# Kernel optimization log

Measured on AMD Instinct MI355X. Metric: run time of the kernel, lower is better.

The kernel has to match this reference:

```python
import jax, jax.numpy as jnp
import numpy as np

B, N, M = 2, 1024, 512
D, H, DH = 1024, 16, 64          # features, heads, head dim (D == H*DH)
MID = H * DH
DC = 768                          # context_features
MULT = 4
EPS = 1e-5


def _ln(x, w, b):
    mu = jnp.mean(x, -1, keepdims=True)
    var = jnp.mean((x - mu) ** 2, -1, keepdims=True)
    return (x - mu) * jax.lax.rsqrt(var + EPS) * w + b


def _sincos(n, d):
    inv = 1.0 / (10000.0 ** (jnp.arange(0, d, 2, dtype=jnp.float32) / d))
    ang = jnp.arange(n, dtype=jnp.float32)[:, None] * inv[None, :]
    return jnp.sin(ang), jnp.cos(ang)


def _rope(x, sin, cos):
    # x: [B,H,N,DH]; sin/cos: [N, DH//2]; interleaved even/odd rotation
    s = sin[None, None]
    c = cos[None, None]
    xe = x[..., ::2]
    xo = x[..., 1::2]
    re = xe * c - xo * s
    ro = xe * s + xo * c
    return jnp.stack((re, ro), axis=-1).reshape(x.shape)


def _heads(t):
    b, n, _ = t.shape
    return t.reshape(b, n, H, DH).transpose(0, 2, 1, 3)


def _attn(xq, ctx, wq, wkv, wo, bo):
    q = _heads(xq @ wq)
    k, v = jnp.split(ctx @ wkv, 2, axis=-1)
    k = _heads(k)
    v = _heads(v)
    sq, cq = _sincos(q.shape[2], DH)
    sk, ck = _sincos(k.shape[2], DH)
    q = _rope(q, sq, cq)
    k = _rope(k, sk, ck)
    sim = jnp.einsum('bhnd,bhmd->bhnm', q, k) * (DH ** -0.5)
    a = jax.nn.softmax(sim, axis=-1)
    o = jnp.einsum('bhnm,bhmd->bhnd', a, v)
    o = o.transpose(0, 2, 1, 3).reshape(xq.shape[0], xq.shape[1], MID)
    return o @ wo + bo


def _adaln(x, c, lw, lb, gw, gb, bw, bb):
    g = (c @ gw + gb)[:, None, :]
    bt = (c @ bw + bb)[:, None, :]
    return _ln(x, lw, lb) * (1.0 + g) + bt


def setup_inputs() -> dict:
    ks = jax.random.split(jax.random.key(0), 24)
    s = 0.02
    inp = {
        'x': jax.random.normal(ks[0], (B, N, D), jnp.float32),
        'cond': jax.random.normal(ks[1], (B, D), jnp.float32),
        'context': jax.random.normal(ks[2], (B, M, DC), jnp.float32),
        # AdaLN (attn_mod) — reused for self- and cross-attention pre-norm
        'ln1_w': jnp.ones((D,), jnp.float32),
        'ln1_b': jnp.zeros((D,), jnp.float32),
        'g1_w': jax.random.normal(ks[3], (D, D), jnp.float32) * s,
        'g1_b': jnp.zeros((D,), jnp.float32),
        'b1_w': jax.random.normal(ks[4], (D, D), jnp.float32) * s,
        'b1_b': jnp.zeros((D,), jnp.float32),
        # AdaLN (ffn_mod)
        'ln2_w': jnp.ones((D,), jnp.float32),
        'ln2_b': jnp.zeros((D,), jnp.float32),
        'g2_w': jax.random.normal(ks[5], (D, D), jnp.float32) * s,
        'g2_b': jnp.zeros((D,), jnp.float32),
        'b2_w': jax.random.normal(ks[6], (D, D), jnp.float32) * s,
        'b2_b': jnp.zeros((D,), jnp.float32),
        # self-attention
        'sa_wq': jax.random.normal(ks[7], (D, MID), jnp.float32) * s,
        'sa_wkv': jax.random.normal(ks[8], (D, 2 * MID), jnp.float32) * s,
        'sa_wo': jax.random.normal(ks[9], (MID, D), jnp.float32) * s,
        'sa_bo': jnp.zeros((D,), jnp.float32),
        # cross-attention (context LayerNorm + projections)
        'ca_lnc_w': jnp.ones((DC,), jnp.float32),
        'ca_lnc_b': jnp.zeros((DC,), jnp.float32),
        'ca_wq': jax.random.normal(ks[10], (D, MID), jnp.float32) * s,
        'ca_wkv': jax.random.normal(ks[11], (DC, 2 * MID), jnp.float32) * s,
        'ca_wo': jax.random.normal(ks[12], (MID, D), jnp.float32) * s,
        'ca_bo': jnp.zeros((D,), jnp.float32),
        # FFN
        'ff_w1': jax.random.normal(ks[13], (D, MULT * D), jnp.float32) * s,
        'ff_b1': jnp.zeros((MULT * D,), jnp.float32),
        'ff_w2': jax.random.normal(ks[14], (MULT * D, D), jnp.float32) * s,
        'ff_b2': jnp.zeros((D,), jnp.float32),
    }
    return inp


def reference(x, cond, context,
              ln1_w, ln1_b, g1_w, g1_b, b1_w, b1_b,
              ln2_w, ln2_b, g2_w, g2_b, b2_w, b2_b,
              sa_wq, sa_wkv, sa_wo, sa_bo,
              ca_lnc_w, ca_lnc_b, ca_wq, ca_wkv, ca_wo, ca_bo,
              ff_w1, ff_b1, ff_w2, ff_b2):
    # self-attention with shared attn_mod AdaLN
    attn_in = _adaln(x, cond, ln1_w, ln1_b, g1_w, g1_b, b1_w, b1_b)
    x = _attn(attn_in, attn_in, sa_wq, sa_wkv, sa_wo, sa_bo) + x
    # cross-attention (attn_mod reused, context LayerNorm applied)
    cross_in = _adaln(x, cond, ln1_w, ln1_b, g1_w, g1_b, b1_w, b1_b)
    ctx_n = _ln(context, ca_lnc_w, ca_lnc_b)
    x = _attn(cross_in, ctx_n, ca_wq, ca_wkv, ca_wo, ca_bo) + x
    # FFN with ffn_mod AdaLN, exact GELU (torch default)
    ffn_in = _adaln(x, cond, ln2_w, ln2_b, g2_w, g2_b, b2_w, b2_b)
    h = jax.nn.gelu(ffn_in @ ff_w1 + ff_b1, approximate=False)
    x = h @ ff_w2 + ff_b2 + x
    return x
```

## Files before the change

kernel.cpp:

```cpp
#include <hip/hip_runtime.h>
#include <hip/hip_bf16.h>
#include <math.h>


typedef float f32x4 __attribute__((ext_vector_type(4)));
typedef __bf16 bf16x8 __attribute__((ext_vector_type(8)));
typedef __bf16 bf16x4 __attribute__((ext_vector_type(4)));
typedef __bf16 bf16x2 __attribute__((ext_vector_type(2)));

#define DEVI __device__ __forceinline__

DEVI void gload16(const void* g, void* l) {
  __builtin_amdgcn_global_load_lds((const __attribute__((address_space(1))) void*)g,
                                   (__attribute__((address_space(3))) void*)l, 16, 0, 0);
}

struct WtDesc {
  const float* src[8];
  __bf16* dst[8];
  int K[8], N[8];
  int tstart[9];
};

__global__ __launch_bounds__(256) void wt_all_kernel(WtDesc d) {
  __shared__ float tile[32][33];
  int blk = blockIdx.x;
  int e = 0;
#pragma unroll
  for (int i = 0; i < 7; ++i) e += (blk >= d.tstart[i + 1]) ? 1 : 0;
  int li = blk - d.tstart[e];
  const float* W = d.src[e];
  __bf16* WT = d.dst[e];
  int K = d.K[e], N = d.N[e];
  int ntx = N >> 5;
  int n0 = (li % ntx) * 32, k0 = (li / ntx) * 32;
  int tx = threadIdx.x & 31, ty = threadIdx.x >> 5;
#pragma unroll
  for (int i = 0; i < 4; ++i) {
    int k = ty + i * 8;
    tile[k][tx] = W[(size_t)(k0 + k) * N + n0 + tx];
  }
  __syncthreads();
#pragma unroll
  for (int i = 0; i < 4; ++i) {
    int n = ty + i * 8;
    WT[(size_t)(n0 + n) * K + k0 + tx] = (__bf16)tile[tx][n];
  }
}

__global__ __launch_bounds__(256) void mod_part_kernel(
    const float* __restrict__ cond,
    const float* __restrict__ g1w, const float* __restrict__ b1w,
    const float* __restrict__ g2w, const float* __restrict__ b2w,
    float* __restrict__ part) {
  __shared__ float sc[128];
  int dchunk = blockIdx.x, b = blockIdx.y;
  int mat = blockIdx.z >> 3, ks = blockIdx.z & 7;
  const float* W = (mat == 0) ? g1w : (mat == 1) ? b1w : (mat == 2) ? g2w : b2w;
  if (threadIdx.x < 128) sc[threadIdx.x] = cond[b * 1024 + ks * 128 + threadIdx.x];
  __syncthreads();
  int d = dchunk * 256 + threadIdx.x;
  const float* Wp = W + (size_t)(ks * 128) * 1024 + d;
  float acc = 0.f;
#pragma unroll 8
  for (int k = 0; k < 128; ++k) acc += sc[k] * Wp[(size_t)k * 1024];
  part[(size_t)(blockIdx.z * 2 + b) * 1024 + d] = acc;
}

__global__ __launch_bounds__(256) void mod_reduce_kernel(
    const float* __restrict__ part,
    const float* __restrict__ g1b, const float* __restrict__ b1b,
    const float* __restrict__ g2b, const float* __restrict__ b2b,
    float* __restrict__ mods) {
  int idx = blockIdx.x * 256 + threadIdx.x;
  int mat = idx >> 11, b = (idx >> 10) & 1, d = idx & 1023;
  float s = 0.f;
#pragma unroll
  for (int ks = 0; ks < 8; ++ks) s += part[(size_t)((mat * 8 + ks) * 2 + b) * 1024 + d];
  const float* Bv = (mat == 0) ? g1b : (mat == 1) ? b1b : (mat == 2) ? g2b : b2b;
  mods[(size_t)(mat * 2 + b) * 1024 + d] = s + Bv[d];
}

__global__ __launch_bounds__(256) void adaln_kernel(const float* __restrict__ X,
                                                    const float* __restrict__ lnw,
                                                    const float* __restrict__ lnb,
                                                    const float* __restrict__ mods,
                                                    int gi, int bi,
                                                    __bf16* __restrict__ out) {
  __shared__ float red[2][4];
  int row = blockIdx.x;
  int b = row >> 10;
  int t = threadIdx.x;
  const float4 xv = ((const float4*)(X + (size_t)row * 1024))[t];
  float s  = xv.x + xv.y + xv.z + xv.w;
  float s2 = xv.x * xv.x + xv.y * xv.y + xv.z * xv.z + xv.w * xv.w;
  int lane = t & 63, w = t >> 6;
#pragma unroll
  for (int off = 32; off > 0; off >>= 1) {
    s += __shfl_down(s, off);
    s2 += __shfl_down(s2, off);
  }
  if (lane == 0) { red[0][w] = s; red[1][w] = s2; }
  __syncthreads();
  s  = red[0][0] + red[0][1] + red[0][2] + red[0][3];
  s2 = red[1][0] + red[1][1] + red[1][2] + red[1][3];
  float mu = s * (1.0f / 1024.0f);
  float var = s2 * (1.0f / 1024.0f) - mu * mu;
  float rstd = rsqrtf(var + 1e-5f);
  const float4 wv = ((const float4*)lnw)[t];
  const float4 bv = ((const float4*)lnb)[t];
  const float4 gv = ((const float4*)(mods + (size_t)(gi * 2 + b) * 1024))[t];
  const float4 tv = ((const float4*)(mods + (size_t)(bi * 2 + b) * 1024))[t];
  bf16x4 ov;
  ov[0] = (__bf16)(((xv.x - mu) * rstd * wv.x + bv.x) * (1.0f + gv.x) + tv.x);
  ov[1] = (__bf16)(((xv.y - mu) * rstd * wv.y + bv.y) * (1.0f + gv.y) + tv.y);
  ov[2] = (__bf16)(((xv.z - mu) * rstd * wv.z + bv.z) * (1.0f + gv.z) + tv.z);
  ov[3] = (__bf16)(((xv.w - mu) * rstd * wv.w + bv.w) * (1.0f + gv.w) + tv.w);
  *(bf16x4*)(out + (size_t)row * 1024 + t * 4) = ov;
}

__global__ __launch_bounds__(256) void ctxln_kernel(const float* __restrict__ X,
                                                    const float* __restrict__ w,
                                                    const float* __restrict__ bias,
                                                    __bf16* __restrict__ out) {
  __shared__ float red[2][4];
  int row = blockIdx.x;
  int t = threadIdx.x;
  const float* xp = X + (size_t)row * 768;
  float v[3];
  float s = 0.f, s2 = 0.f;
#pragma unroll
  for (int i = 0; i < 3; ++i) {
    v[i] = xp[t + i * 256];
    s += v[i];
    s2 += v[i] * v[i];
  }
  int lane = t & 63, wv_ = t >> 6;
#pragma unroll
  for (int off = 32; off > 0; off >>= 1) {
    s += __shfl_down(s, off);
    s2 += __shfl_down(s2, off);
  }
  if (lane == 0) { red[0][wv_] = s; red[1][wv_] = s2; }
  __syncthreads();
  s  = red[0][0] + red[0][1] + red[0][2] + red[0][3];
  s2 = red[1][0] + red[1][1] + red[1][2] + red[1][3];
  float mu = s * (1.0f / 768.0f);
  float var = s2 * (1.0f / 768.0f) - mu * mu;
  float rstd = rsqrtf(var + 1e-5f);
#pragma unroll
  for (int i = 0; i < 3; ++i) {
    int c = t + i * 256;
    out[(size_t)row * 768 + c] = (__bf16)((v[i] - mu) * rstd * w[c] + bias[c]);
  }
}

__global__ __launch_bounds__(256) void rope_tbl_kernel(float2* __restrict__ tbl) {
  int idx = blockIdx.x * 256 + threadIdx.x;
  int n = idx >> 5, i = idx & 31;
  float inv = expf(-(float)(2 * i) * (1.0f / 64.0f) * 9.210340371976184f);
  float ang = (float)n * inv;
  tbl[idx] = make_float2(sinf(ang), cosf(ang));
}

__global__ __launch_bounds__(256) void rope_kernel(const float* __restrict__ X, int ldx, int col0,
                                                   const float2* __restrict__ tbl,
                                                   __bf16* __restrict__ out, int Ntok, float scale) {
  int idx = blockIdx.x * 256 + threadIdx.x;
  int i = idx & 31;
  int h = (idx >> 5) & 15;
  int nn = idx >> 9;
  int n = nn % Ntok;
  int b = nn / Ntok;
  const float* xp = X + (size_t)(b * Ntok + n) * ldx + col0 + h * 64 + 2 * i;
  float xe = xp[0], xo = xp[1];
  float2 sc2 = tbl[n * 32 + i];
  float re = (xe * sc2.y - xo * sc2.x) * scale;
  float ro = (xe * sc2.x + xo * sc2.y) * scale;
  __bf16* op = out + ((size_t)(b * 16 + h) * Ntok + n) * 64 + 2 * i;
  op[0] = (__bf16)re;
  op[1] = (__bf16)ro;
}

__global__ __launch_bounds__(256) void vt_kernel(const float* __restrict__ KV, int ld, int col0,
                                                 __bf16* __restrict__ VT, int Ntok) {
  __shared__ float tile[32][33];
  int bh = blockIdx.x;
  int n0 = blockIdx.y * 32, d0 = blockIdx.z * 32;
  int b = bh >> 4, h = bh & 15;
  int tx = threadIdx.x & 31, ty = threadIdx.x >> 5;
#pragma unroll
  for (int i = 0; i < 4; ++i) {
    int n = ty + i * 8;
    tile[n][tx] = KV[(size_t)(b * Ntok + n0 + n) * ld + col0 + h * 64 + d0 + tx];
  }
  __syncthreads();
#pragma unroll
  for (int i = 0; i < 4; ++i) {
    int d = ty + i * 8;
    VT[((size_t)bh * 64 + d0 + d) * Ntok + n0 + tx] = (__bf16)tile[tx][d];
  }
}

template <int BM, int BN, int EPI>
__global__ __launch_bounds__(256) void gemm3(const __bf16* __restrict__ A,
                                             const __bf16* __restrict__ BT,
                                             const float* __restrict__ bias,
                                             const float* __restrict__ res,
                                             void* __restrict__ outv,
                                             int M, int N, int K, int kslices) {
  constexpr int MI = BM / 32, NI = BN / 32;
  __shared__ __bf16 sA[2][BM * 32];
  __shared__ __bf16 sB[2][BN * 32];
  const int t = threadIdx.x;
  const int w = t >> 6, lane = t & 63;
  const int lr = lane & 15, lg = lane >> 4;
  const int fxor = (lr >> 1) & 3;
  int nwg = gridDim.x * gridDim.y * gridDim.z;
  int flat = blockIdx.x + gridDim.x * (blockIdx.y + gridDim.y * blockIdx.z);
  flat = (flat & 7) * (nwg >> 3) + (flat >> 3);
  const int bm = flat % gridDim.x;
  int rest = flat / gridDim.x;
  const int bn = rest % gridDim.y;
  const int bz = rest / gridDim.y;
  const int wm = (w >> 1) * (BM / 2), wn = (w & 1) * (BN / 2);
  const int kper = K / kslices;
  const int k0 = bz * kper;
  f32x4 acc[MI][NI] = {};

  auto stage = [&](int buf, int kt) {
#pragma unroll
    for (int i = 0; i < BM / 64; ++i) {
      int e8 = i * 256 + t;
      int row = e8 >> 2, c = e8 & 3;
      int scol = (c ^ ((row >> 1) & 3)) << 3;
      gload16(A + (size_t)(bm * BM + row) * K + kt + scol, &sA[buf][e8 * 8]);
    }
#pragma unroll
    for (int i = 0; i < BN / 64; ++i) {
      int e8 = i * 256 + t;
      int row = e8 >> 2, c = e8 & 3;
      int scol = (c ^ ((row >> 1) & 3)) << 3;
      gload16(BT + (size_t)(bn * BN + row) * K + kt + scol, &sB[buf][e8 * 8]);
    }
  };

  stage(0, k0);
  __syncthreads();
  int cur = 0;
  for (int kt = k0; kt < k0 + kper; kt += 32) {
    if (kt + 32 < k0 + kper) stage(cur ^ 1, kt + 32);
    bf16x8 af[MI], bfr[NI];
#pragma unroll
    for (int mi = 0; mi < MI; ++mi)
      af[mi] = *(const bf16x8*)(&sA[cur][(wm + mi * 16 + lr) * 32 + ((lg ^ fxor) << 3)]);
#pragma unroll
    for (int ni = 0; ni < NI; ++ni)
      bfr[ni] = *(const bf16x8*)(&sB[cur][(wn + ni * 16 + lr) * 32 + ((lg ^ fxor) << 3)]);
#pragma unroll
    for (int mi = 0; mi < MI; ++mi)
#pragma unroll
      for (int ni = 0; ni < NI; ++ni)
        acc[mi][ni] = __builtin_amdgcn_mfma_f32_16x16x32_bf16(af[mi], bfr[ni], acc[mi][ni], 0, 0, 0);
    __syncthreads();
    cur ^= 1;
  }
#pragma unroll
  for (int mi = 0; mi < MI; ++mi) {
    int row = bm * BM + wm + mi * 16 + lg * 4;
#pragma unroll
    for (int ni = 0; ni < NI; ++ni) {
      int col = bn * BN + wn + ni * 16 + lr;
#pragma unroll
      for (int r = 0; r < 4; ++r) {
        float v = acc[mi][ni][r];
        size_t off = (size_t)(row + r) * N + col;
        if (EPI == 0) {
          ((float*)outv)[off] = v;
        } else if (EPI == 1) {
          ((float*)outv)[off] = v + bias[col] + res[off];
        } else if (EPI == 2) {
          float xg = v + bias[col];
          ((__bf16*)outv)[off] = (__bf16)(0.5f * xg * (1.0f + erff(xg * 0.7071067811865475f)));
        } else {
          ((float*)outv)[(size_t)bz * M * N + off] = v;
        }
      }
    }
  }
}

__global__ __launch_bounds__(256) void ff2red_kernel(const float* __restrict__ part,
                                                     const float* __restrict__ bias,
                                                     const float* __restrict__ res,
                                                     float* __restrict__ out, int MN, int N) {
  int idx = blockIdx.x * 256 + threadIdx.x;
  float4 p0 = ((const float4*)part)[idx];
  float4 p1 = ((const float4*)(part + MN))[idx];
  float4 rr = ((const float4*)res)[idx];
  int colb = (idx * 4) & (N - 1);
  float4 bb = *(const float4*)(bias + colb);
  float4 o;
  o.x = p0.x + p1.x + bb.x + rr.x;
  o.y = p0.y + p1.y + bb.y + rr.y;
  o.z = p0.z + p1.z + bb.z + rr.z;
  o.w = p0.w + p1.w + bb.w + rr.w;
  ((float4*)out)[idx] = o;
}

template <int KITERS>
__global__ __launch_bounds__(256) void attn_part_kernel(const __bf16* __restrict__ Qr,
                                                        const __bf16* __restrict__ Kr,
                                                        const __bf16* __restrict__ VT,
                                                        float* __restrict__ pO,
                                                        float* __restrict__ pml,
                                                        int Nq, int Nk) {
  __shared__ __bf16 sK[2][64 * 64];
  __shared__ __bf16 sV[2][64 * 64];
  __shared__ __bf16 Pl[4][16 * 64];
  const int t = threadIdx.x, w = t >> 6, lane = t & 63;
  const int lr = lane & 15, lg = lane >> 4;
  const int lsrc = lane & 48;
  const int swz = (lr & 7) << 3;
  int flat = blockIdx.x + (blockIdx.y << 4) + (blockIdx.z << 9);
  flat = (flat & 7) * 128 + (flat >> 3);
  const int bh = (flat >> 4) & 31, z = flat >> 9;
  const int q0 = (flat & 15) * 64 + w * 16;
  const int k0 = z * (KITERS * 64);

  auto stage = [&](int buf, int kt) {
#pragma unroll
    for (int i = 0; i < 2; ++i) {
      int e8 = i * 256 + t;
      int row = e8 >> 3, col8 = e8 & 7;
      int scol = (col8 ^ (row & 7)) << 3;
      gload16(Kr + ((size_t)bh * Nk + kt + row) * 64 + scol, &sK[buf][e8 * 8]);
      gload16(VT + ((size_t)bh * 64 + row) * Nk + kt + scol, &sV[buf][e8 * 8]);
    }
  };

  bf16x8 qf[2];
#pragma unroll
  for (int kh = 0; kh < 2; ++kh)
    qf[kh] = *(const bf16x8*)(Qr + ((size_t)bh * Nq + q0 + lr) * 64 + kh * 32 + lg * 8);
  f32x4 accO[4] = {};
  float m = -INFINITY, l = 0.f;

  stage(0, k0);
  __syncthreads();
  int cur = 0;
#pragma unroll
  for (int it = 0; it < KITERS; ++it) {
    if (it + 1 < KITERS) stage(cur ^ 1, k0 + (it + 1) * 64);
    f32x4 s[4] = {};
#pragma unroll
    for (int nf = 0; nf < 4; ++nf) {
      int r = nf * 16 + lr;
#pragma unroll
      for (int kh = 0; kh < 2; ++kh) {
        bf16x8 kf = *(const bf16x8*)(&sK[cur][r * 64 + (((kh * 4 + lg) ^ (lr & 7)) << 3)]);
        s[nf] = __builtin_amdgcn_mfma_f32_16x16x32_bf16(kf, qf[kh], s[nf], 0, 0, 0);
      }
    }
    float p[16];
#pragma unroll
    for (int j = 0; j < 16; ++j) p[j] = s[j >> 2][j & 3];
    float pm = p[0];
#pragma unroll
    for (int j = 1; j < 16; ++j) pm = fmaxf(pm, p[j]);
    pm = fmaxf(pm, __shfl_xor(pm, 16));
    pm = fmaxf(pm, __shfl_xor(pm, 32));
    if (!__all(pm <= m + 8.f)) {
      float mnew = fmaxf(m, pm);
      float resc = __expf(m - mnew);
      float rq[4];
#pragma unroll
      for (int r = 0; r < 4; ++r) rq[r] = __shfl(resc, lsrc | (lg * 4 + r));
#pragma unroll
      for (int df = 0; df < 4; ++df)
#pragma unroll
        for (int r = 0; r < 4; ++r) accO[df][r] *= rq[r];
      l *= resc;
      m = mnew;
    }
    float rs = 0.f;
#pragma unroll
    for (int j = 0; j < 16; ++j) { p[j] = __expf(p[j] - m); rs += p[j]; }
    rs += __shfl_xor(rs, 16);
    rs += __shfl_xor(rs, 32);
    l += rs;
#pragma unroll
    for (int nf = 0; nf < 4; ++nf)
#pragma unroll
      for (int jj = 0; jj < 2; ++jj) {
        int k = nf * 16 + lg * 4 + 2 * jj;
        bf16x2 pk;
        pk[0] = (__bf16)p[nf * 4 + 2 * jj];
        pk[1] = (__bf16)p[nf * 4 + 2 * jj + 1];
        *(bf16x2*)(&Pl[w][lr * 64 + (k ^ swz)]) = pk;
      }
    bf16x8 pa0 = *(const bf16x8*)(&Pl[w][lr * 64 + ((lg * 8) ^ swz)]);
    bf16x8 pa1 = *(const bf16x8*)(&Pl[w][lr * 64 + ((32 + lg * 8) ^ swz)]);
#pragma unroll
    for (int df = 0; df < 4; ++df) {
      int d = df * 16 + lr;
      bf16x8 vf0 = *(const bf16x8*)(&sV[cur][d * 64 + ((lg ^ (lr & 7)) << 3)]);
      bf16x8 vf1 = *(const bf16x8*)(&sV[cur][d * 64 + (((4 + lg) ^ (lr & 7)) << 3)]);
      accO[df] = __builtin_amdgcn_mfma_f32_16x16x32_bf16(pa0, vf0, accO[df], 0, 0, 0);
      accO[df] = __builtin_amdgcn_mfma_f32_16x16x32_bf16(pa1, vf1, accO[df], 0, 0, 0);
    }
    __syncthreads();
    cur ^= 1;
  }
  const size_t rbase = (size_t)(z * 32 + bh) * Nq + q0;
  if (lg == 0) {
    pml[(rbase + lr) * 2] = m;
    pml[(rbase + lr) * 2 + 1] = l;
  }
#pragma unroll
  for (int r = 0; r < 4; ++r)
#pragma unroll
    for (int df = 0; df < 4; ++df)
      pO[(rbase + lg * 4 + r) * 64 + df * 16 + lr] = accO[df][r];
}

__global__ __launch_bounds__(256) void attn_combine_kernel(const float* __restrict__ pO,
                                                           const float* __restrict__ pml,
                                                           __bf16* __restrict__ O) {
  int idx = blockIdx.x * 256 + threadIdx.x;
  int r = idx >> 6, dh = idx & 63;
  float m0 = pml[2 * r], l0 = pml[2 * r + 1];
  float m1 = pml[2 * (r + 32768)], l1 = pml[2 * (r + 32768) + 1];
  float O0 = pO[(size_t)r * 64 + dh];
  float O1 = pO[((size_t)r + 32768) * 64 + dh];
  float mm = fmaxf(m0, m1);
  float w0 = __expf(m0 - mm), w1 = __expf(m1 - mm);
  float val = (O0 * w0 + O1 * w1) / (l0 * w0 + l1 * w1);
  int bh = r >> 10, n = r & 1023;
  int b = bh >> 4, h = bh & 15;
  O[(size_t)(b * 1024 + n) * 1024 + h * 64 + dh] = (__bf16)val;
}

extern "C" void kernel_launch(void* const* d_in, const int* in_sizes, int n_in,
                              void* d_out, int out_size, void* d_ws, size_t ws_size,
                              hipStream_t stream) {
  (void)in_sizes; (void)n_in; (void)out_size; (void)ws_size;
  const float* x       = (const float*)d_in[0];
  const float* cond    = (const float*)d_in[1];
  const float* ctx     = (const float*)d_in[2];
  const float* ln1_w   = (const float*)d_in[3];
  const float* ln1_b   = (const float*)d_in[4];
  const float* g1_w    = (const float*)d_in[5];
  const float* g1_b    = (const float*)d_in[6];
  const float* b1_w    = (const float*)d_in[7];
  const float* b1_b    = (const float*)d_in[8];
  const float* ln2_w   = (const float*)d_in[9];
  const float* ln2_b   = (const float*)d_in[10];
  const float* g2_w    = (const float*)d_in[11];
  const float* g2_b    = (const float*)d_in[12];
  const float* b2_w    = (const float*)d_in[13];
  const float* b2_b    = (const float*)d_in[14];
  const float* sa_wq   = (const float*)d_in[15];
  const float* sa_wkv  = (const float*)d_in[16];
  const float* sa_wo   = (const float*)d_in[17];
  const float* sa_bo   = (const float*)d_in[18];
  const float* ca_lnc_w = (const float*)d_in[19];
  const float* ca_lnc_b = (const float*)d_in[20];
  const float* ca_wq   = (const float*)d_in[21];
  const float* ca_wkv  = (const float*)d_in[22];
  const float* ca_wo   = (const float*)d_in[23];
  const float* ca_bo   = (const float*)d_in[24];
  const float* ff_w1   = (const float*)d_in[25];
  const float* ff_b1   = (const float*)d_in[26];
  const float* ff_w2   = (const float*)d_in[27];
  const float* ff_b2   = (const float*)d_in[28];
  float* out = (float*)d_out;

  char* ws = (char*)d_ws;
  size_t o = 0;
  auto alloc = [&](size_t bytes) {
    void* p = ws + o;
    o += (bytes + 255) & ~(size_t)255;
    return p;
  };

  __bf16* wqT   = (__bf16*)alloc(1024ull * 1024 * 2);
  __bf16* wkvT  = (__bf16*)alloc(2048ull * 1024 * 2);
  __bf16* woT   = (__bf16*)alloc(1024ull * 1024 * 2);
  __bf16* cwqT  = (__bf16*)alloc(1024ull * 1024 * 2);
  __bf16* cwkvT = (__bf16*)alloc(2048ull * 768 * 2);
  __bf16* cwoT  = (__bf16*)alloc(1024ull * 1024 * 2);
  __bf16* ff1T  = (__bf16*)alloc(4096ull * 1024 * 2);
  __bf16* ff2T  = (__bf16*)alloc(1024ull * 4096 * 2);
  float*  mods  = (float*)alloc(4ull * 2 * 1024 * 4);
  float2* tbl   = (float2*)alloc(1024ull * 32 * 8);
  __bf16* ain   = (__bf16*)alloc(2048ull * 1024 * 2);
  float*  Qf    = (float*)alloc(2048ull * 1024 * 4);
  float*  KVf   = (float*)alloc(2048ull * 2048 * 4);
  __bf16* ctxn  = (__bf16*)alloc(1024ull * 768 * 2);
  __bf16* Qr    = (__bf16*)alloc(2048ull * 1024 * 2);
  __bf16* Kr    = (__bf16*)alloc(2048ull * 1024 * 2);
  __bf16* VTb   = (__bf16*)alloc(2048ull * 1024 * 2);
  __bf16* Ob    = (__bf16*)alloc(2048ull * 1024 * 2);
  float*  x1    = (float*)alloc(2048ull * 1024 * 4);
  float*  x2    = (float*)alloc(2048ull * 1024 * 4);
  float*  QKVf  = Qf;
  __bf16* hb    = (__bf16*)KVf;
  float*  pbuf  = (float*)Qr;
  float*  mpart = (float*)Qf;
  float*  pO    = (float*)KVf;
  float*  pml   = (float*)Qf;

  WtDesc wd;
  const float* srcs[8] = {sa_wq, sa_wkv, sa_wo, ca_wq, ca_wkv, ca_wo, ff_w1, ff_w2};
  __bf16* dsts[8] = {wqT, wkvT, woT, cwqT, cwkvT, cwoT, ff1T, ff2T};
  int Ks[8] = {1024, 1024, 1024, 1024, 768, 1024, 1024, 4096};
  int Ns[8] = {1024, 2048, 1024, 1024, 2048, 1024, 4096, 1024};
  int cum = 0;
  for (int i = 0; i < 8; ++i) {
    wd.src[i] = srcs[i]; wd.dst[i] = dsts[i]; wd.K[i] = Ks[i]; wd.N[i] = Ns[i];
    wd.tstart[i] = cum;
    cum += (Ks[i] >> 5) * (Ns[i] >> 5);
  }
  wd.tstart[8] = cum;
  wt_all_kernel<<<cum, 256, 0, stream>>>(wd);
  rope_tbl_kernel<<<128, 256, 0, stream>>>(tbl);
  mod_part_kernel<<<dim3(4, 2, 32), 256, 0, stream>>>(cond, g1_w, b1_w, g2_w, b2_w, mpart);
  mod_reduce_kernel<<<32, 256, 0, stream>>>(mpart, g1_b, b1_b, g2_b, b2_b, mods);

  adaln_kernel<<<2048, 256, 0, stream>>>(x, ln1_w, ln1_b, mods, 0, 1, ain);
  gemm3<128, 64, 0><<<dim3(16, 48), 256, 0, stream>>>(ain, wqT, nullptr, nullptr, QKVf, 2048, 3072, 1024, 1);
  rope_kernel<<<4096, 256, 0, stream>>>(QKVf, 3072, 0, tbl, Qr, 1024, 0.125f);
  rope_kernel<<<4096, 256, 0, stream>>>(QKVf, 3072, 1024, tbl, Kr, 1024, 1.0f);
  vt_kernel<<<dim3(32, 32, 2), 256, 0, stream>>>(QKVf, 3072, 2048, VTb, 1024);
  attn_part_kernel<8><<<dim3(16, 32, 2), 256, 0, stream>>>(Qr, Kr, VTb, pO, pml, 1024, 1024);
  attn_combine_kernel<<<8192, 256, 0, stream>>>(pO, pml, Ob);
  gemm3<128, 64, 1><<<dim3(16, 16), 256, 0, stream>>>(Ob, woT, sa_bo, x, x1, 2048, 1024, 1024, 1);

  adaln_kernel<<<2048, 256, 0, stream>>>(x1, ln1_w, ln1_b, mods, 0, 1, ain);
  ctxln_kernel<<<1024, 256, 0, stream>>>(ctx, ca_lnc_w, ca_lnc_b, ctxn);
  gemm3<128, 64, 0><<<dim3(16, 16), 256, 0, stream>>>(ain, cwqT, nullptr, nullptr, Qf, 2048, 1024, 1024, 1);
  gemm3<64, 128, 0><<<dim3(16, 16), 256, 0, stream>>>(ctxn, cwkvT, nullptr, nullptr, KVf, 1024, 2048, 768, 1);
  rope_kernel<<<4096, 256, 0, stream>>>(Qf, 1024, 0, tbl, Qr, 1024, 0.125f);
  rope_kernel<<<2048, 256, 0, stream>>>(KVf, 2048, 0, tbl, Kr, 512, 1.0f);
  vt_kernel<<<dim3(32, 16, 2), 256, 0, stream>>>(KVf, 2048, 1024, VTb, 512);
  attn_part_kernel<4><<<dim3(16, 32, 2), 256, 0, stream>>>(Qr, Kr, VTb, pO, pml, 1024, 512);
  attn_combine_kernel<<<8192, 256, 0, stream>>>(pO, pml, Ob);
  gemm3<128, 64, 1><<<dim3(16, 16), 256, 0, stream>>>(Ob, cwoT, ca_bo, x1, x2, 2048, 1024, 1024, 1);

  adaln_kernel<<<2048, 256, 0, stream>>>(x2, ln2_w, ln2_b, mods, 2, 3, ain);
  gemm3<128, 128, 2><<<dim3(16, 32), 256, 0, stream>>>(ain, ff1T, ff_b1, nullptr, hb, 2048, 4096, 1024, 1);
  gemm3<128, 64, 3><<<dim3(16, 16, 2), 256, 0, stream>>>(hb, ff2T, nullptr, nullptr, pbuf, 2048, 1024, 4096, 2);
  ff2red_kernel<<<2048, 256, 0, stream>>>(pbuf, ff_b2, x2, out, 2048 * 1024, 1024);
}
```

Measured before the change: 285.2 us.

## Deepen GEMM global-to-LDS pipeline with multi-buffer prefetch and explicit vmcnt waits

Rewrites the gemm3 main loop to keep several k-tiles in flight, using NBUF=DEPTH+1 LDS buffers. It waits with a partial s_waitcnt vmcnt and issues a single barrier per iteration instead of a full double-buffer sync. The aim is to hide global load latency behind MFMA work. The cross-attention KV GEMM also moves from a 64x128 to a 128x64 tile. The extra buffers raise LDS use per block, which may lower occupancy, and the hand-written vmcnt counting depends on each thread issuing exactly LPT loads per stage.

```diff
diff --git a/kernel.cpp b/kernel.cpp
--- a/kernel.cpp
+++ b/kernel.cpp
@@ -202,7 +202,7 @@
   }
 }
 
-template <int BM, int BN, int EPI>
+template <int BM, int BN, int EPI, int DEPTH>
 __global__ __launch_bounds__(256) void gemm3(const __bf16* __restrict__ A,
                                              const __bf16* __restrict__ BT,
                                              const float* __restrict__ bias,
@@ -210,8 +210,10 @@
                                              void* __restrict__ outv,
                                              int M, int N, int K, int kslices) {
   constexpr int MI = BM / 32, NI = BN / 32;
-  __shared__ __bf16 sA[2][BM * 32];
-  __shared__ __bf16 sB[2][BN * 32];
+  constexpr int NBUF = DEPTH + 1;
+  constexpr int LPT = BM / 64 + BN / 64;
+  __shared__ __bf16 sA[NBUF][BM * 32];
+  __shared__ __bf16 sB[NBUF][BN * 32];
   const int t = threadIdx.x;
   const int w = t >> 6, lane = t & 63;
   const int lr = lane & 15, lg = lane >> 4;
@@ -226,6 +228,7 @@
   const int wm = (w >> 1) * (BM / 2), wn = (w & 1) * (BN / 2);
   const int kper = K / kslices;
   const int k0 = bz * kper;
+  const int nsteps = kper / 32;
   f32x4 acc[MI][NI] = {};
 
   auto stage = [&](int buf, int kt) {
@@ -245,26 +248,37 @@
     }
   };
 
-  stage(0, k0);
-  __syncthreads();
-  int cur = 0;
-  for (int kt = k0; kt < k0 + kper; kt += 32) {
-    if (kt + 32 < k0 + kper) stage(cur ^ 1, kt + 32);
+  auto compute = [&](int buf) {
     bf16x8 af[MI], bfr[NI];
 #pragma unroll
     for (int mi = 0; mi < MI; ++mi)
-      af[mi] = *(const bf16x8*)(&sA[cur][(wm + mi * 16 + lr) * 32 + ((lg ^ fxor) << 3)]);
+      af[mi] = *(const bf16x8*)(&sA[buf][(wm + mi * 16 + lr) * 32 + ((lg ^ fxor) << 3)]);
 #pragma unroll
     for (int ni = 0; ni < NI; ++ni)
-      bfr[ni] = *(const bf16x8*)(&sB[cur][(wn + ni * 16 + lr) * 32 + ((lg ^ fxor) << 3)]);
+      bfr[ni] = *(const bf16x8*)(&sB[buf][(wn + ni * 16 + lr) * 32 + ((lg ^ fxor) << 3)]);
 #pragma unroll
     for (int mi = 0; mi < MI; ++mi)
 #pragma unroll
       for (int ni = 0; ni < NI; ++ni)
         acc[mi][ni] = __builtin_amdgcn_mfma_f32_16x16x32_bf16(af[mi], bfr[ni], acc[mi][ni], 0, 0, 0);
-    __syncthreads();
-    cur ^= 1;
-  }
+  };
+
+#pragma unroll
+  for (int i = 0; i < DEPTH; ++i) stage(i, k0 + i * 32);
+
+  int it = 0;
+  for (; it < nsteps - (DEPTH - 1); ++it) {
+    asm volatile("s_waitcnt vmcnt(%0)" :: "n"((DEPTH - 1) * LPT) : "memory");
+    __builtin_amdgcn_s_barrier();
+    __builtin_amdgcn_sched_barrier(0);
+    if (it + DEPTH < nsteps) stage((it + DEPTH) % NBUF, k0 + (it + DEPTH) * 32);
+    compute(it % NBUF);
+  }
+  asm volatile("s_waitcnt vmcnt(0)" ::: "memory");
+  __builtin_amdgcn_s_barrier();
+  __builtin_amdgcn_sched_barrier(0);
+  for (; it < nsteps; ++it) compute(it % NBUF);
+
 #pragma unroll
   for (int mi = 0; mi < MI; ++mi) {
     int row = bm * BM + wm + mi * 16 + lg * 4;
@@ -529,27 +543,27 @@
   mod_reduce_kernel<<<32, 256, 0, stream>>>(mpart, g1_b, b1_b, g2_b, b2_b, mods);
 
   adaln_kernel<<<2048, 256, 0, stream>>>(x, ln1_w, ln1_b, mods, 0, 1, ain);
-  gemm3<128, 64, 0><<<dim3(16, 48), 256, 0, stream>>>(ain, wqT, nullptr, nullptr, QKVf, 2048, 3072, 1024, 1);
+  gemm3<128, 64, 0, 3><<<dim3(16, 48), 256, 0, stream>>>(ain, wqT, nullptr, nullptr, QKVf, 2048, 3072, 1024, 1);
   rope_kernel<<<4096, 256, 0, stream>>>(QKVf, 3072, 0, tbl, Qr, 1024, 0.125f);
   rope_kernel<<<4096, 256, 0, stream>>>(QKVf, 3072, 1024, tbl, Kr, 1024, 1.0f);
   vt_kernel<<<dim3(32, 32, 2), 256, 0, stream>>>(QKVf, 3072, 2048, VTb, 1024);
   attn_part_kernel<8><<<dim3(16, 32, 2), 256, 0, stream>>>(Qr, Kr, VTb, pO, pml, 1024, 1024);
   attn_combine_kernel<<<8192, 256, 0, stream>>>(pO, pml, Ob);
-  gemm3<128, 64, 1><<<dim3(16, 16), 256, 0, stream>>>(Ob, woT, sa_bo, x, x1, 2048, 1024, 1024, 1);
+  gemm3<128, 64, 1, 3><<<dim3(16, 16), 256, 0, stream>>>(Ob, woT, sa_bo, x, x1, 2048, 1024, 1024, 1);
 
   adaln_kernel<<<2048, 256, 0, stream>>>(x1, ln1_w, ln1_b, mods, 0, 1, ain);
   ctxln_kernel<<<1024, 256, 0, stream>>>(ctx, ca_lnc_w, ca_lnc_b, ctxn);
-  gemm3<128, 64, 0><<<dim3(16, 16), 256, 0, stream>>>(ain, cwqT, nullptr, nullptr, Qf, 2048, 1024, 1024, 1);
-  gemm3<64, 128, 0><<<dim3(16, 16), 256, 0, stream>>>(ctxn, cwkvT, nullptr, nullptr, KVf, 1024, 2048, 768, 1);
+  gemm3<128, 64, 0, 3><<<dim3(16, 16), 256, 0, stream>>>(ain, cwqT, nullptr, nullptr, Qf, 2048, 1024, 1024, 1);
+  gemm3<128, 64, 0, 3><<<dim3(8, 32), 256, 0, stream>>>(ctxn, cwkvT, nullptr, nullptr, KVf, 1024, 2048, 768, 1);
   rope_kernel<<<4096, 256, 0, stream>>>(Qf, 1024, 0, tbl, Qr, 1024, 0.125f);
   rope_kernel<<<2048, 256, 0, stream>>>(KVf, 2048, 0, tbl, Kr, 512, 1.0f);
   vt_kernel<<<dim3(32, 16, 2), 256, 0, stream>>>(KVf, 2048, 1024, VTb, 512);
   attn_part_kernel<4><<<dim3(16, 32, 2), 256, 0, stream>>>(Qr, Kr, VTb, pO, pml, 1024, 512);
   attn_combine_kernel<<<8192, 256, 0, stream>>>(pO, pml, Ob);
-  gemm3<128, 64, 1><<<dim3(16, 16), 256, 0, stream>>>(Ob, cwoT, ca_bo, x1, x2, 2048, 1024, 1024, 1);
+  gemm3<128, 64, 1, 3><<<dim3(16, 16), 256, 0, stream>>>(Ob, cwoT, ca_bo, x1, x2, 2048, 1024, 1024, 1);
 
   adaln_kernel<<<2048, 256, 0, stream>>>(x2, ln2_w, ln2_b, mods, 2, 3, ain);
-  gemm3<128, 128, 2><<<dim3(16, 32), 256, 0, stream>>>(ain, ff1T, ff_b1, nullptr, hb, 2048, 4096, 1024, 1);
-  gemm3<128, 64, 3><<<dim3(16, 16, 2), 256, 0, stream>>>(hb, ff2T, nullptr, nullptr, pbuf, 2048, 1024, 4096, 2);
+  gemm3<128, 128, 2, 2><<<dim3(16, 32), 256, 0, stream>>>(ain, ff1T, ff_b1, nullptr, hb, 2048, 4096, 1024, 1);
+  gemm3<128, 64, 3, 3><<<dim3(16, 16, 2), 256, 0, stream>>>(hb, ff2T, nullptr, nullptr, pbuf, 2048, 1024, 4096, 2);
   ff2red_kernel<<<2048, 256, 0, stream>>>(pbuf, ff_b2, x2, out, 2048 * 1024, 1024);
 }
```

Result: no change. 280.6 us (-1.6%).
